# Optimization experiments

Hardware: AMD Instinct MI355X
Metric: run time of the kernel (lower is better)

## Reference

```python
import jax, jax.numpy as jnp
import numpy as np
import math

B, S, D, H = 4, 512, 1024, 16
DH = D // H
DQ = D // 4
MIN_STEPS, MAX_STEPS = 4, 12
THR = 1e-4


def lin(t, w, b):
    # torch Linear convention: w is (out, in)
    return jnp.einsum('...i,oi->...o', t, w) + b


def gelu(t):
    return jax.nn.gelu(t, approximate=False)  # torch nn.GELU() exact


def layernorm(t, g, b):
    m = t.mean(-1, keepdims=True)
    v = jnp.mean(jnp.square(t - m), axis=-1, keepdims=True)
    return (t - m) * jax.lax.rsqrt(v + 1e-5) * g + b


def _forward(h, x, ig_w1, ig_b1, ig_w2, ig_b2, wq, bq, wk, bk, wv, bv, wo, bo,
             g1_w1, g1_b1, g1_w2, g1_b2, gate_logits, ln_g, ln_b,
             sp_w1, sp_b1, sp_w2, sp_b2):
    # adaptive step count: steps = base + floor(sigmoid(MLP(mean_pool(h))).mean() * extra)
    pooled = h.mean(axis=1)  # (B, D)
    extra = jax.nn.sigmoid(lin(gelu(lin(pooled, sp_w1, sp_b1)), sp_w2, sp_b2)).mean()
    num_steps = jnp.minimum(
        MIN_STEPS + jnp.floor(extra * (MAX_STEPS - MIN_STEPS)).astype(jnp.int32), MAX_STEPS)

    gw = jax.nn.softmax(gate_logits)  # gate weights over the 3 gates
    scale = 1.0 / math.sqrt(DH)

    def step(carry, i):
        h, active = carry
        # G1 gate (G2/G3 multiply zero memory/expert outputs -> drop)
        G1 = jax.nn.sigmoid(lin(gelu(lin(h, g1_w1, g1_b1)), g1_w2, g1_b2)) * gw[0]
        # Phi: input-gated blend + raw multi-head self-attention
        gate = jax.nn.sigmoid(
            lin(gelu(lin(jnp.concatenate([h, x], axis=-1), ig_w1, ig_b1)), ig_w2, ig_b2))
        blended = gate * h + (1.0 - gate) * x
        q = lin(blended, wq, bq).reshape(B, S, H, DH)
        k = lin(blended, wk, bk).reshape(B, S, H, DH)
        v = lin(blended, wv, bv).reshape(B, S, H, DH)
        attn = jax.nn.softmax(jnp.einsum('bqhd,bkhd->bhqk', q, k) * scale, axis=-1)
        ctx = jnp.einsum('bhqk,bkhd->bqhd', attn, v).reshape(B, S, D)
        phi = lin(ctx, wo, bo)
        h_new = layernorm(h + G1 * phi, ln_g, ln_b)
        res = jnp.linalg.norm(h_new - h) / (jnp.linalg.norm(h) + 1e-8)
        act_i = active & (i < num_steps)
        h = jnp.where(act_i, h_new, h)
        active = act_i & jnp.logical_not((i >= MIN_STEPS) & (res < THR))
        return (h, active), None

    (h, _), _ = jax.lax.scan(step, (h, jnp.array(True)), jnp.arange(MAX_STEPS))
    return h


def setup_inputs() -> dict:
    key = jax.random.key(0)
    ks = jax.random.split(key, 16)
    f32 = jnp.float32

    def W(k, out_d, in_d):
        return jax.random.normal(k, (out_d, in_d), f32) * (1.0 / np.sqrt(in_d))

    return {
        'h': jax.random.normal(ks[0], (B, S, D), f32),
        'x': jax.random.normal(ks[1], (B, S, D), f32),
        # PhiLayer input_gate: Linear(2D, D/4) -> GELU -> Linear(D/4, D) -> Sigmoid
        'ig_w1': W(ks[2], DQ, 2 * D), 'ig_b1': jnp.zeros((DQ,), f32),
        'ig_w2': W(ks[3], D, DQ), 'ig_b2': jnp.zeros((D,), f32),
        # QKV / out projections (xavier-ish, zero bias)
        'wq': W(ks[4], D, D), 'bq': jnp.zeros((D,), f32),
        'wk': W(ks[5], D, D), 'bk': jnp.zeros((D,), f32),
        'wv': W(ks[6], D, D), 'bv': jnp.zeros((D,), f32),
        'wo': W(ks[7], D, D), 'bo': jnp.zeros((D,), f32),
        # Gating gate #1 MLP (only G1 contributes; memory/experts are zero)
        'g1_w1': W(ks[8], DQ, D), 'g1_b1': jnp.zeros((DQ,), f32),
        'g1_w2': W(ks[9], D, DQ), 'g1_b2': jnp.zeros((D,), f32),
        'gate_logits': jnp.ones((3,), f32),  # nn.Parameter(torch.ones(3))
        # LayerNorm
        'ln_g': jnp.ones((D,), f32), 'ln_b': jnp.zeros((D,), f32),
        # step predictor: Linear(D, D/4) -> GELU -> Linear(D/4, 1)
        'sp_w1': W(ks[10], DQ, D), 'sp_b1': jnp.zeros((DQ,), f32),
        'sp_w2': W(ks[11], 1, DQ), 'sp_b2': jnp.zeros((1,), f32),
    }


def reference(h, x, ig_w1, ig_b1, ig_w2, ig_b2, wq, bq, wk, bk, wv, bv, wo, bo,
              g1_w1, g1_b1, g1_w2, g1_b2, gate_logits, ln_g, ln_b,
              sp_w1, sp_b1, sp_w2, sp_b2):
    return _forward(h, x, ig_w1, ig_b1, ig_w2, ig_b2, wq, bq, wk, bk, wv, bv, wo, bo,
                    g1_w1, g1_b1, g1_w2, g1_b2, gate_logits, ln_g, ln_b,
                    sp_w1, sp_b1, sp_w2, sp_b2)
```

## Files before the change

kernel.cpp:

```cpp
#include <hip/hip_runtime.h>
#include <hip/hip_bf16.h>


#define B_   4
#define S_   512
#define D_   1024
#define H_   16
#define DH_  64
#define MSEQ 2048
#define GRID_ 512

typedef short short8 __attribute__((ext_vector_type(8)));
typedef float floatx4 __attribute__((ext_vector_type(4)));

static constexpr size_t OFF_H    = 0;
static constexpr size_t OFF_X    = 2097152;
static constexpr size_t OFF_HXB  = 4194304;
static constexpr size_t OFF_T2B  = 6291456;
static constexpr size_t OFF_T1B  = 6553600;
static constexpr size_t OFF_G1B  = 6815744;
static constexpr size_t OFF_QKVB = 7864320;
static constexpr size_t OFF_U    = 7864320;
static constexpr size_t OFF_CTXB = 11010048;
static constexpr size_t OFF_WARE = 12058624;
static constexpr size_t OFF_BIAS = 14811136;
static constexpr size_t OFF_POOL = 14817792;
static constexpr size_t OFF_SPT  = 14821888;
static constexpr size_t OFF_PPART= 14822912;
static constexpr size_t OFF_SCAL = 14888448;
static constexpr size_t OFF_XIG  = 14888960;

static constexpr int W_WIG1 = 0;
static constexpr int W_WIG2 = 524288;
static constexpr int W_WG1  = 786432;
static constexpr int W_WG2  = 1048576;
static constexpr int W_QKV  = 1310720;
static constexpr int W_WO   = 4456448;
static constexpr int W_TOT  = 5505024;
static constexpr int B_TOT  = 6656;

__device__ __forceinline__ float bf2f(unsigned int u) {
  return __uint_as_float((u & 0xFFFFu) << 16);
}
__device__ __forceinline__ short f2bs(float f) {
  __hip_bfloat16 b = __float2bfloat16(f);
  return *reinterpret_cast<short*>(&b);
}
__device__ __forceinline__ unsigned int pk2(float lo, float hi) {
  return (unsigned int)(unsigned short)f2bs(lo) | ((unsigned int)(unsigned short)f2bs(hi) << 16);
}
__device__ __forceinline__ float ldf(const void* p, size_t i, int f32m) {
  return f32m ? ((const float*)p)[i] : bf2f(((const unsigned short*)p)[i]);
}
__device__ __forceinline__ int f32mode(const void* lng) {
  return (((const unsigned int*)lng)[0] == 0x3F800000u) ? 1 : 0;
}
__device__ __forceinline__ float gelu_f(float x) {
  return 0.5f * x * (1.0f + erff(x * 0.70710678118654752440f));
}
__device__ __forceinline__ float sig_f(float x) {
  return 1.0f / (1.0f + expf(-x));
}
__device__ __forceinline__ void gl_lds16(const short* gp, short* lp) {
  __builtin_amdgcn_global_load_lds(
      (const __attribute__((address_space(1))) unsigned int*)gp,
      (__attribute__((address_space(3))) unsigned int*)lp, 16, 0, 0);
}
__device__ __forceinline__ float wave_sum(float v) {
  #pragma unroll
  for (int off = 32; off > 0; off >>= 1) v += __shfl_xor(v, off);
  return v;
}

struct RepackPtrs {
  const void* w[8];
  const void* b[8];
};

__global__ __launch_bounds__(256) void repack_all_kernel(
    const void* __restrict__ lng, RepackPtrs ps,
    short* __restrict__ wdst, float* __restrict__ bdst) {
  const int f32m = f32mode(lng);
  int i = blockIdx.x * 256 + threadIdx.x;
  if (i < W_TOT) {
    const int off[9] = {0, 524288, 786432, 1048576, 1310720, 2359296, 3407872, 4456448, W_TOT};
    int seg = 0;
    #pragma unroll
    for (int s = 1; s < 8; s++) seg += (i >= off[s]) ? 1 : 0;
    wdst[i] = f2bs(ldf(ps.w[seg], i - off[seg], f32m));
  } else if (i < W_TOT + B_TOT) {
    int j = i - W_TOT;
    const int off[9] = {0, 256, 1280, 1536, 2560, 3584, 4608, 5632, B_TOT};
    int seg = 0;
    #pragma unroll
    for (int s = 1; s < 8; s++) seg += (j >= off[s]) ? 1 : 0;
    bdst[j] = ldf(ps.b[seg], j - off[seg], f32m);
  }
}

__global__ __launch_bounds__(256) void cvt_in_kernel(
    const void* __restrict__ lng, const void* __restrict__ hb,
    const void* __restrict__ xb, float* __restrict__ h, float* __restrict__ x,
    short* __restrict__ hxb, int n) {
  int f32m = f32mode(lng);
  int i = blockIdx.x * 256 + threadIdx.x;
  if (i < n) {
    float hv = ldf(hb, i, f32m);
    float xv = ldf(xb, i, f32m);
    h[i] = hv;
    x[i] = xv;
    int row = i >> 10, col = i & 1023;
    hxb[(size_t)row * 2048 + col] = f2bs(hv);
    hxb[(size_t)row * 2048 + 1024 + col] = f2bs(xv);
  }
}

__global__ __launch_bounds__(256) void pool_s1_kernel(
    const float* __restrict__ H, float* __restrict__ part) {
  int b = blockIdx.x, c = blockIdx.y, tid = threadIdx.x;
  const float* p = H + ((size_t)b * S_ + c * 32) * D_;
  #pragma unroll
  for (int rep = 0; rep < 4; rep++) {
    int d = rep * 256 + tid;
    float s = 0.f;
    for (int r = 0; r < 32; r++) s += p[(size_t)r * D_ + d];
    part[((size_t)b * 16 + c) * D_ + d] = s;
  }
}
__global__ __launch_bounds__(256) void pool_s2_kernel(
    const float* __restrict__ part, float* __restrict__ pooled) {
  int i = blockIdx.x * 256 + threadIdx.x;
  int b = i >> 10, d = i & 1023;
  float s = 0.f;
  #pragma unroll
  for (int c = 0; c < 16; c++) s += part[((size_t)b * 16 + c) * D_ + d];
  pooled[i] = s * (1.0f / (float)S_);
}

__device__ __forceinline__ float blk_sum256(float v, float* sm, int tid) {
  #pragma unroll
  for (int off = 32; off > 0; off >>= 1) v += __shfl_xor(v, off);
  __syncthreads();
  if ((tid & 63) == 0) sm[tid >> 6] = v;
  __syncthreads();
  return sm[0] + sm[1] + sm[2] + sm[3];
}

__global__ __launch_bounds__(256) void sp1_kernel(
    const void* __restrict__ lng, const float* __restrict__ pooled,
    const void* __restrict__ w1, const void* __restrict__ b1,
    float* __restrict__ spt) {
  __shared__ float sm[4];
  const int f32m = f32mode(lng);
  int j = blockIdx.x, tid = threadIdx.x;
  float s[4] = {0.f, 0.f, 0.f, 0.f};
  #pragma unroll
  for (int r = 0; r < 4; r++) {
    int k = tid * 4 + r;
    float w = ldf(w1, (size_t)j * D_ + k, f32m);
    s[0] += pooled[k] * w;
    s[1] += pooled[1024 + k] * w;
    s[2] += pooled[2048 + k] * w;
    s[3] += pooled[3072 + k] * w;
  }
  #pragma unroll
  for (int b = 0; b < 4; b++) {
    float t = blk_sum256(s[b], sm, tid);
    __syncthreads();
    if (tid == 0) spt[b * 256 + j] = gelu_f(t + ldf(b1, j, f32m));
  }
}

__global__ __launch_bounds__(256) void sp2_kernel(
    const void* __restrict__ lng, const float* __restrict__ spt,
    const void* __restrict__ w2, const void* __restrict__ b2,
    const void* __restrict__ glog,
    int* __restrict__ num_steps, int* __restrict__ active, int* __restrict__ cur,
    float* __restrict__ gw0, float* __restrict__ ssd, float* __restrict__ ssh,
    int* __restrict__ cnt) {
  __shared__ float z[4];
  const int f32m = f32mode(lng);
  int tid = threadIdx.x;
  if (tid < 12) cnt[tid] = 0;
  int wave = tid >> 6, lane = tid & 63;
  {
    int b = wave;
    float s = spt[b * 256 + lane]       * ldf(w2, lane, f32m) +
              spt[b * 256 + lane + 64]  * ldf(w2, lane + 64, f32m) +
              spt[b * 256 + lane + 128] * ldf(w2, lane + 128, f32m) +
              spt[b * 256 + lane + 192] * ldf(w2, lane + 192, f32m);
    #pragma unroll
    for (int off = 32; off > 0; off >>= 1) s += __shfl_xor(s, off);
    if (lane == 0) z[b] = sig_f(s + ldf(b2, 0, f32m));
  }
  __syncthreads();
  if (tid == 0) {
    float extra = 0.25f * (z[0] + z[1] + z[2] + z[3]);
    int ns = 4 + (int)floorf(extra * 8.0f);
    if (ns > 12) ns = 12;
    *num_steps = ns;
    *active = 1;
    *cur = 1;
    *ssd = 0.f; *ssh = 0.f;
    float g0 = ldf(glog, 0, f32m);
    float g1 = ldf(glog, 1, f32m);
    float g2 = ldf(glog, 2, f32m);
    float mx = fmaxf(g0, fmaxf(g1, g2));
    float e0 = expf(g0 - mx), e1 = expf(g1 - mx), e2 = expf(g2 - mx);
    *gw0 = e0 / (e0 + e1 + e2);
  }
}

enum { EPI_NONE = 0, EPI_GELU = 1, EPI_SIGSCALE = 2, EPI_BLEND = 3, EPI_RESADD = 4,
       EPI_GELU_ADD = 5, EPI_F32NB = 6 };

template <int EPI, int BM, int BN>
__device__ __forceinline__ void mgemm_core(
    short* As, short* Bs,
    const short* __restrict__ A, int lda,
    const short* __restrict__ W, int ldw, const float* __restrict__ bias,
    int K, int N,
    float* __restrict__ Cf, short* __restrict__ Cb,
    const float* __restrict__ aux1, const float* __restrict__ aux2f,
    const short* __restrict__ aux2b, const float* __restrict__ scale_ptr,
    int m0, int n0) {
  constexpr int FM = (BM / 2) / 16;
  constexpr int FN = (BN / 2) / 16;
  constexpr int CPA = (BM / 16) / 4;
  constexpr int CPB = (BN / 16) / 4;
  const int tid = threadIdx.x;
  const int lane = tid & 63, wv_ = tid >> 6;
  const int wm = (wv_ >> 1) * (BM / 2), wn = (wv_ & 1) * (BN / 2);
  const int srow = lane >> 2, scol = (lane & 3) * 8;
  const int frow = lane & 15, fk = (lane >> 4) * 8;

  floatx4 acc[FM][FN];
  #pragma unroll
  for (int i = 0; i < FM; i++)
    #pragma unroll
    for (int j = 0; j < FN; j++) acc[i][j] = (floatx4){0.f, 0.f, 0.f, 0.f};

  for (int k0 = 0; k0 < K; k0 += 64) {
    __syncthreads();
    #pragma unroll
    for (int c = 0; c < CPA; c++) {
      int q = wv_ * CPA + c;
      const short* gp = A + (size_t)(m0 + q * 16 + srow) * lda + k0 + scol;
      gl_lds16(gp, As + q * 512);
      gl_lds16(gp + 32, As + BM * 32 + q * 512);
    }
    #pragma unroll
    for (int c = 0; c < CPB; c++) {
      int q = wv_ * CPB + c;
      const short* gp = W + (size_t)(n0 + q * 16 + srow) * ldw + k0 + scol;
      gl_lds16(gp, Bs + q * 512);
      gl_lds16(gp + 32, Bs + BN * 32 + q * 512);
    }
    __syncthreads();
    #pragma unroll
    for (int hlf = 0; hlf < 2; hlf++) {
      const short* Ah = As + hlf * BM * 32;
      const short* Bh = Bs + hlf * BN * 32;
      short8 a[FM], b[FN];
      #pragma unroll
      for (int i = 0; i < FM; i++)
        a[i] = *reinterpret_cast<const short8*>(&Ah[(wm + i * 16 + frow) * 32 + fk]);
      #pragma unroll
      for (int j = 0; j < FN; j++)
        b[j] = *reinterpret_cast<const short8*>(&Bh[(wn + j * 16 + frow) * 32 + fk]);
      #pragma unroll
      for (int i = 0; i < FM; i++)
        #pragma unroll
        for (int j = 0; j < FN; j++)
          acc[i][j] = __builtin_amdgcn_mfma_f32_16x16x32_bf16(a[i], b[j], acc[i][j], 0, 0, 0);
    }
  }

  float gwv = 0.f;
  if (EPI == EPI_SIGSCALE) gwv = *scale_ptr;
  const int rq = (lane >> 4) * 4;
  #pragma unroll
  for (int i = 0; i < FM; i++) {
    #pragma unroll
    for (int j = 0; j < FN; j++) {
      int n = n0 + wn + j * 16 + (lane & 15);
      float bv = (EPI == EPI_F32NB) ? 0.f : bias[n];
      #pragma unroll
      for (int r = 0; r < 4; r++) {
        int m = m0 + wm + i * 16 + rq + r;
        size_t off = (size_t)m * N + n;
        float v = acc[i][j][r] + bv;
        if (EPI == EPI_GELU) {
          Cb[off] = f2bs(gelu_f(v));
        } else if (EPI == EPI_GELU_ADD) {
          if (aux1) v += aux1[off];
          Cb[off] = f2bs(gelu_f(v));
        } else if (EPI == EPI_SIGSCALE) {
          Cb[off] = f2bs(sig_f(v) * gwv);
        } else if (EPI == EPI_BLEND) {
          float s = sig_f(v);
          Cb[off] = f2bs(s * aux1[off] + (1.f - s) * aux2f[off]);
        } else if (EPI == EPI_RESADD) {
          Cf[off] = aux1[off] + bf2f((unsigned short)aux2b[off]) * v;
        } else if (EPI == EPI_F32NB) {
          Cf[off] = v;
        } else {
          Cb[off] = f2bs(v);
        }
      }
    }
  }
}

template <int EPI, int BM, int BN>
__global__ __launch_bounds__(256) void mgemm(
    const int* __restrict__ flag, const short* __restrict__ A, int lda,
    const short* __restrict__ W, int ldw, const float* __restrict__ bias,
    int K, int N,
    float* __restrict__ Cf, short* __restrict__ Cb,
    const float* __restrict__ aux1, const float* __restrict__ aux2f,
    const short* __restrict__ aux2b, const float* __restrict__ scale_ptr) {
  if (flag && *flag == 0) return;
  __shared__ short As[BM * 64];
  __shared__ short Bs[BN * 64];
  mgemm_core<EPI, BM, BN>(As, Bs, A, lda, W, ldw, bias, K, N, Cf, Cb,
                          aux1, aux2f, aux2b, scale_ptr,
                          blockIdx.y * BM, blockIdx.x * BN);
}

__global__ __launch_bounds__(256) void gate1_kernel(
    const int* __restrict__ flag, const short* __restrict__ hxb,
    const short* __restrict__ warena, const float* __restrict__ biasA,
    short* __restrict__ t2b, short* __restrict__ t1b,
    const float* __restrict__ xig, int kz0) {
  if (*flag == 0) return;
  __shared__ short As[64 * 64];
  __shared__ short Bs[64 * 64];
  if (blockIdx.z == 0)
    mgemm_core<EPI_GELU_ADD, 64, 64>(As, Bs, hxb, 2048, warena + W_WIG1, 2048,
                                     biasA + 0, kz0, 256, nullptr, t2b, xig,
                                     nullptr, nullptr, nullptr,
                                     blockIdx.y * 64, blockIdx.x * 64);
  else
    mgemm_core<EPI_GELU, 64, 64>(As, Bs, hxb, 2048, warena + W_WG1, 1024,
                                 biasA + 1280, 1024, 256, nullptr, t1b, nullptr,
                                 nullptr, nullptr, nullptr,
                                 blockIdx.y * 64, blockIdx.x * 64);
}

__global__ __launch_bounds__(256) void gate2_kernel(
    const int* __restrict__ flag, const short* __restrict__ t2b,
    const short* __restrict__ t1b, const short* __restrict__ warena,
    const float* __restrict__ biasA, short* __restrict__ bldb,
    short* __restrict__ g1b, const float* __restrict__ h,
    const float* __restrict__ xf, const float* __restrict__ gw0) {
  if (*flag == 0) return;
  __shared__ short As[128 * 64];
  __shared__ short Bs[64 * 64];
  if (blockIdx.z == 0)
    mgemm_core<EPI_BLEND, 128, 64>(As, Bs, t2b, 256, warena + W_WIG2, 256,
                                   biasA + 256, 256, 1024, nullptr, bldb, h, xf,
                                   nullptr, nullptr, blockIdx.y * 128, blockIdx.x * 64);
  else
    mgemm_core<EPI_SIGSCALE, 128, 64>(As, Bs, t1b, 256, warena + W_WG2, 256,
                                      biasA + 1536, 256, 1024, nullptr, g1b,
                                      nullptr, nullptr, nullptr, gw0,
                                      blockIdx.y * 128, blockIdx.x * 64);
}

#define AP_ 72
__global__ __launch_bounds__(256) void attn_kernel(
    const int* __restrict__ flag, const short* __restrict__ qkv,
    short* __restrict__ ctxb) {
  if (*flag == 0) return;
  __shared__ short Ks[64 * AP_];
  __shared__ short Vt[64 * AP_];
  __shared__ short Ps[64 * AP_];
  const int tid = threadIdx.x;
  const int lane = tid & 63, wv = tid >> 6;
  const int ln15 = lane & 15, quad = lane >> 4;
  const int qt = blockIdx.x, hh = blockIdx.y, b = blockIdx.z;
  const int wm = wv * 16;
  const size_t rowbase = (size_t)b * S_;
  const int hcol = hh * DH_;
  const float scale = 0.125f;

  short8 qa[2];
  {
    const short* qp = qkv + (rowbase + qt * 64 + wm + ln15) * 3072 + hcol + quad * 8;
    qa[0] = *reinterpret_cast<const short8*>(qp);
    qa[1] = *reinterpret_cast<const short8*>(qp + 32);
  }
  const int skk = tid >> 2, scg = (tid & 3) * 16;

  float mrow[4] = {-1e30f, -1e30f, -1e30f, -1e30f};
  float lrow[4] = {0.f, 0.f, 0.f, 0.f};
  floatx4 accO[4];
  #pragma unroll
  for (int j = 0; j < 4; j++) accO[j] = (floatx4){0.f, 0.f, 0.f, 0.f};

  for (int kt = 0; kt < 8; kt++) {
    __syncthreads();
    {
      const short* gk = qkv + (rowbase + kt * 64 + skk) * 3072 + 1024 + hcol + scg;
      uint4 k0 = *reinterpret_cast<const uint4*>(gk);
      uint4 k1 = *reinterpret_cast<const uint4*>(gk + 8);
      *reinterpret_cast<uint4*>(&Ks[skk * AP_ + scg]) = k0;
      *reinterpret_cast<uint4*>(&Ks[skk * AP_ + scg + 8]) = k1;
      short8 v0 = *reinterpret_cast<const short8*>(gk + 1024);
      short8 v1 = *reinterpret_cast<const short8*>(gk + 1032);
      #pragma unroll
      for (int j = 0; j < 8; j++) Vt[(scg + j) * AP_ + skk] = v0[j];
      #pragma unroll
      for (int j = 0; j < 8; j++) Vt[(scg + 8 + j) * AP_ + skk] = v1[j];
    }
    __syncthreads();

    floatx4 sc[4];
    #pragma unroll
    for (int nf = 0; nf < 4; nf++) {
      short8 b0 = *reinterpret_cast<const short8*>(&Ks[(nf * 16 + ln15) * AP_ + quad * 8]);
      short8 b1 = *reinterpret_cast<const short8*>(&Ks[(nf * 16 + ln15) * AP_ + 32 + quad * 8]);
      floatx4 s = (floatx4){0.f, 0.f, 0.f, 0.f};
      s = __builtin_amdgcn_mfma_f32_16x16x32_bf16(qa[0], b0, s, 0, 0, 0);
      s = __builtin_amdgcn_mfma_f32_16x16x32_bf16(qa[1], b1, s, 0, 0, 0);
      sc[nf] = s;
    }

    float prob[4][4];
    #pragma unroll
    for (int r = 0; r < 4; r++) {
      float lm = fmaxf(fmaxf(sc[0][r], sc[1][r]), fmaxf(sc[2][r], sc[3][r])) * scale;
      lm = fmaxf(lm, __shfl_xor(lm, 1));
      lm = fmaxf(lm, __shfl_xor(lm, 2));
      lm = fmaxf(lm, __shfl_xor(lm, 4));
      lm = fmaxf(lm, __shfl_xor(lm, 8));
      float mn = fmaxf(mrow[r], lm);
      float alpha = expf(mrow[r] - mn);
      float ls = 0.f;
      #pragma unroll
      for (int nf = 0; nf < 4; nf++) {
        float p = expf(sc[nf][r] * scale - mn);
        prob[nf][r] = p;
        ls += p;
      }
      ls += __shfl_xor(ls, 1);
      ls += __shfl_xor(ls, 2);
      ls += __shfl_xor(ls, 4);
      ls += __shfl_xor(ls, 8);
      lrow[r] = lrow[r] * alpha + ls;
      mrow[r] = mn;
      #pragma unroll
      for (int df = 0; df < 4; df++) accO[df][r] *= alpha;
    }
    #pragma unroll
    for (int nf = 0; nf < 4; nf++)
      #pragma unroll
      for (int r = 0; r < 4; r++)
        Ps[(wm + quad * 4 + r) * AP_ + nf * 16 + ln15] = f2bs(prob[nf][r]);
    __syncthreads();

    short8 pa0 = *reinterpret_cast<const short8*>(&Ps[(wm + ln15) * AP_ + quad * 8]);
    short8 pa1 = *reinterpret_cast<const short8*>(&Ps[(wm + ln15) * AP_ + 32 + quad * 8]);
    #pragma unroll
    for (int df = 0; df < 4; df++) {
      short8 bv0 = *reinterpret_cast<const short8*>(&Vt[(df * 16 + ln15) * AP_ + quad * 8]);
      short8 bv1 = *reinterpret_cast<const short8*>(&Vt[(df * 16 + ln15) * AP_ + 32 + quad * 8]);
      accO[df] = __builtin_amdgcn_mfma_f32_16x16x32_bf16(pa0, bv0, accO[df], 0, 0, 0);
      accO[df] = __builtin_amdgcn_mfma_f32_16x16x32_bf16(pa1, bv1, accO[df], 0, 0, 0);
    }
  }

  float inv[4];
  #pragma unroll
  for (int r = 0; r < 4; r++) inv[r] = 1.0f / lrow[r];
  #pragma unroll
  for (int df = 0; df < 4; df++) {
    #pragma unroll
    for (int r = 0; r < 4; r++) {
      size_t off = (rowbase + qt * 64 + wm + quad * 4 + r) * 1024 + hcol + df * 16 + ln15;
      ctxb[off] = f2bs(accO[df][r] * inv[r]);
    }
  }
}

__global__ __launch_bounds__(256) void ln_kernel(
    int step_i, const int* __restrict__ flagp,
    const float* __restrict__ U, float* __restrict__ H, short* __restrict__ hxb,
    const void* __restrict__ g, const void* __restrict__ be,
    void* __restrict__ Out,
    float* __restrict__ ssd, float* __restrict__ ssh,
    int* __restrict__ active, int* __restrict__ cur,
    const int* __restrict__ num_steps, int* __restrict__ cnt) {
  const int flag = *flagp;
  const int f32m = f32mode(g);
  __shared__ float sdd[4], sdh[4];
  const int tid = threadIdx.x;
  const int wv = tid >> 6, lane = tid & 63;
  if (flag) {
    const int row = blockIdx.x * 4 + wv;
    const float4* u4 = reinterpret_cast<const float4*>(U + (size_t)row * D_);
    float4* h4 = reinterpret_cast<float4*>(H + (size_t)row * D_);
    float4 uv[4], hv[4];
    #pragma unroll
    for (int j = 0; j < 4; j++) uv[j] = u4[lane + 64 * j];
    #pragma unroll
    for (int j = 0; j < 4; j++) hv[j] = h4[lane + 64 * j];
    float s = 0.f;
    #pragma unroll
    for (int j = 0; j < 4; j++) s += (uv[j].x + uv[j].y) + (uv[j].z + uv[j].w);
    s = wave_sum(s);
    float mean = s * (1.0f / (float)D_);
    float4 d[4];
    float vv = 0.f;
    #pragma unroll
    for (int j = 0; j < 4; j++) {
      d[j].x = uv[j].x - mean; d[j].y = uv[j].y - mean;
      d[j].z = uv[j].z - mean; d[j].w = uv[j].w - mean;
      vv += d[j].x * d[j].x + d[j].y * d[j].y + d[j].z * d[j].z + d[j].w * d[j].w;
    }
    vv = wave_sum(vv);
    float rstd = rsqrtf(vv * (1.0f / (float)D_) + 1e-5f);
    float lsd = 0.f, lsh = 0.f;
    #pragma unroll
    for (int j = 0; j < 4; j++) {
      int c = (lane + 64 * j) * 4;
      float hn0 = d[j].x * rstd * ldf(g, c + 0, f32m) + ldf(be, c + 0, f32m);
      float hn1 = d[j].y * rstd * ldf(g, c + 1, f32m) + ldf(be, c + 1, f32m);
      float hn2 = d[j].z * rstd * ldf(g, c + 2, f32m) + ldf(be, c + 2, f32m);
      float hn3 = d[j].w * rstd * ldf(g, c + 3, f32m) + ldf(be, c + 3, f32m);
      float e0 = hn0 - hv[j].x, e1 = hn1 - hv[j].y, e2 = hn2 - hv[j].z, e3 = hn3 - hv[j].w;
      lsd += e0 * e0 + e1 * e1 + e2 * e2 + e3 * e3;
      lsh += hv[j].x * hv[j].x + hv[j].y * hv[j].y + hv[j].z * hv[j].z + hv[j].w * hv[j].w;
      float4 hnv = make_float4(hn0, hn1, hn2, hn3);
      h4[lane + 64 * j] = hnv;
      uint2 pw;
      pw.x = pk2(hn0, hn1);
      pw.y = pk2(hn2, hn3);
      *reinterpret_cast<uint2*>(hxb + (size_t)row * 2048 + c) = pw;
      if (f32m) {
        reinterpret_cast<float4*>(Out)[(size_t)row * 256 + lane + 64 * j] = hnv;
      } else {
        *reinterpret_cast<uint2*>((short*)Out + (size_t)row * 1024 + c) = pw;
      }
    }
    lsd = wave_sum(lsd);
    lsh = wave_sum(lsh);
    if (lane == 0) { sdd[wv] = lsd; sdh[wv] = lsh; }
    __syncthreads();
    if (tid == 0) {
      atomicAdd(ssd, (sdd[0] + sdd[1]) + (sdd[2] + sdd[3]));
      atomicAdd(ssh, (sdh[0] + sdh[1]) + (sdh[2] + sdh[3]));
    }
  }
  if (tid == 0) {
    __threadfence();
    int old = atomicAdd(&cnt[step_i], 1);
    if (old == (int)gridDim.x - 1) {
      if (flag && step_i >= 4) {
        float nd = atomicAdd(ssd, 0.0f);
        float nh = atomicAdd(ssh, 0.0f);
        float res = sqrtf(nd) / (sqrtf(nh) + 1e-8f);
        if (res < 1e-4f) *active = 0;
      }
      *cur = ((*active) && (step_i + 1 < *num_steps)) ? 1 : 0;
      *ssd = 0.f; *ssh = 0.f;
    }
  }
}

extern "C" void kernel_launch(void* const* d_in, const int* in_sizes, int n_in,
                              void* d_out, int out_size, void* d_ws, size_t ws_size,
                              hipStream_t stream) {
  (void)in_sizes; (void)n_in; (void)out_size;
  const void* h_in  = d_in[0];
  const void* x_in  = d_in[1];
  const void* glog  = d_in[18];
  const void* ln_g  = d_in[19];
  const void* ln_b  = d_in[20];
  const void* sp_w1 = d_in[21];
  const void* sp_b1 = d_in[22];
  const void* sp_w2 = d_in[23];
  const void* sp_b2 = d_in[24];

  RepackPtrs rp;
  rp.w[0] = d_in[2];  rp.w[1] = d_in[4];  rp.w[2] = d_in[14]; rp.w[3] = d_in[16];
  rp.w[4] = d_in[6];  rp.w[5] = d_in[8];  rp.w[6] = d_in[10]; rp.w[7] = d_in[12];
  rp.b[0] = d_in[3];  rp.b[1] = d_in[5];  rp.b[2] = d_in[15]; rp.b[3] = d_in[17];
  rp.b[4] = d_in[7];  rp.b[5] = d_in[9];  rp.b[6] = d_in[11]; rp.b[7] = d_in[13];

  float* wsf = (float*)d_ws;
  float* h      = wsf + OFF_H;
  float* xf     = wsf + OFF_X;
  short* hxb    = (short*)(wsf + OFF_HXB);
  short* t2b    = (short*)(wsf + OFF_T2B);
  short* t1b    = (short*)(wsf + OFF_T1B);
  short* g1b    = (short*)(wsf + OFF_G1B);
  short* qkvb   = (short*)(wsf + OFF_QKVB);
  float* u      = wsf + OFF_U;
  short* ctxb   = (short*)(wsf + OFF_CTXB);
  short* bldb   = ctxb;
  short* warena = (short*)(wsf + OFF_WARE);
  float* biasA  = wsf + OFF_BIAS;
  float* pooled = wsf + OFF_POOL;
  float* spt    = wsf + OFF_SPT;
  float* ppart  = wsf + OFF_PPART;
  float* xigf   = wsf + OFF_XIG;
  float* ssd    = wsf + OFF_SCAL + 0;
  float* ssh    = wsf + OFF_SCAL + 1;
  float* gw0    = wsf + OFF_SCAL + 2;
  int* ip        = (int*)(wsf + OFF_SCAL + 8);
  int* num_steps = ip + 0;
  int* active    = ip + 1;
  int* cur       = ip + 2;
  int* cnt       = ip + 4;

  const int NTOT = B_ * S_ * D_;

  const int use_xig = (ws_size >= (OFF_XIG + 524288) * sizeof(float)) ? 1 : 0;
  const int kz0 = use_xig ? 1024 : 2048;

  repack_all_kernel<<<(W_TOT + B_TOT + 255) / 256, 256, 0, stream>>>(ln_g, rp, warena, biasA);
  cvt_in_kernel<<<NTOT / 256, 256, 0, stream>>>(ln_g, h_in, x_in, h, xf, hxb, NTOT);
  if (use_xig) {
    mgemm<EPI_F32NB, 64, 64><<<dim3(4, 32), 256, 0, stream>>>(
        nullptr, hxb + 1024, 2048, warena + W_WIG1 + 1024, 2048, nullptr,
        1024, 256, xigf, nullptr, nullptr, nullptr, nullptr, nullptr);
  }
  pool_s1_kernel<<<dim3(4, 16), 256, 0, stream>>>(h, ppart);
  pool_s2_kernel<<<16, 256, 0, stream>>>(ppart, pooled);
  sp1_kernel<<<256, 256, 0, stream>>>(ln_g, pooled, sp_w1, sp_b1, spt);
  sp2_kernel<<<1, 256, 0, stream>>>(ln_g, spt, sp_w2, sp_b2, glog,
                                    num_steps, active, cur, gw0, ssd, ssh, cnt);

  for (int i = 0; i < 12; i++) {
    gate1_kernel<<<dim3(4, 32, 2), 256, 0, stream>>>(
        cur, hxb, warena, biasA, t2b, t1b, use_xig ? xigf : nullptr, kz0);
    gate2_kernel<<<dim3(16, 16, 2), 256, 0, stream>>>(cur, t2b, t1b, warena, biasA,
                                                      bldb, g1b, h, xf, gw0);
    mgemm<EPI_NONE, 128, 64><<<dim3(48, 16), 256, 0, stream>>>(
        cur, bldb, 1024, warena + W_QKV, 1024, biasA + 2560, 1024, 3072,
        nullptr, qkvb, nullptr, nullptr, nullptr, nullptr);
    attn_kernel<<<dim3(8, 16, 4), 256, 0, stream>>>(cur, qkvb, ctxb);
    mgemm<EPI_RESADD, 64, 64><<<dim3(16, 32), 256, 0, stream>>>(
        cur, ctxb, 1024, warena + W_WO, 1024, biasA + 5632, 1024, 1024,
        u, nullptr, h, nullptr, g1b, nullptr);
    ln_kernel<<<512, 256, 0, stream>>>(i, cur, u, h, hxb, ln_g, ln_b, d_out,
                                       ssd, ssh, active, cur, num_steps, cnt);
  }
}
```

Measured before the change: 1.201 ms.

## Enlarge attention query tile to 128 rows with transposed MFMA and packed stores

The attention kernel now runs 8 waves per block over 128 query rows, so each K/V tile staged in LDS is shared by twice as many waves and global K/V reloads are halved. The per-wave P buffer no longer needs a block barrier before it is read back, so one __syncthreads is dropped. The PV MFMA operand order is swapped to produce a transposed accumulator, with alpha and the row sums redistributed by lane shuffles, which allows 8-byte packed bf16 stores of the context. The trade-off is half as many blocks in the grid, which means less parallelism across CUs.

Result: no change. 1.214 ms (+1.0%).

```diff
diff --git a/kernel.cpp b/kernel.cpp
--- a/kernel.cpp
+++ b/kernel.cpp
@@ -369,13 +369,13 @@
 }
 
 #define AP_ 72
-__global__ __launch_bounds__(256) void attn_kernel(
+__global__ __launch_bounds__(512) void attn_kernel(
     const int* __restrict__ flag, const short* __restrict__ qkv,
     short* __restrict__ ctxb) {
   if (*flag == 0) return;
   __shared__ short Ks[64 * AP_];
   __shared__ short Vt[64 * AP_];
-  __shared__ short Ps[64 * AP_];
+  __shared__ short Ps[128 * AP_];
   const int tid = threadIdx.x;
   const int lane = tid & 63, wv = tid >> 6;
   const int ln15 = lane & 15, quad = lane >> 4;
@@ -384,14 +384,16 @@
   const size_t rowbase = (size_t)b * S_;
   const int hcol = hh * DH_;
   const float scale = 0.125f;
+  const int srcl = ((ln15 >> 2) << 4) + ln15;
+  const int rsel = ln15 & 3;
 
   short8 qa[2];
   {
-    const short* qp = qkv + (rowbase + qt * 64 + wm + ln15) * 3072 + hcol + quad * 8;
+    const short* qp = qkv + (rowbase + qt * 128 + wm + ln15) * 3072 + hcol + quad * 8;
     qa[0] = *reinterpret_cast<const short8*>(qp);
     qa[1] = *reinterpret_cast<const short8*>(qp + 32);
   }
-  const int skk = tid >> 2, scg = (tid & 3) * 16;
+  const int skk = tid >> 3, scg = (tid & 7) * 8;
 
   float mrow[4] = {-1e30f, -1e30f, -1e30f, -1e30f};
   float lrow[4] = {0.f, 0.f, 0.f, 0.f};
@@ -404,15 +406,10 @@
     {
       const short* gk = qkv + (rowbase + kt * 64 + skk) * 3072 + 1024 + hcol + scg;
       uint4 k0 = *reinterpret_cast<const uint4*>(gk);
-      uint4 k1 = *reinterpret_cast<const uint4*>(gk + 8);
       *reinterpret_cast<uint4*>(&Ks[skk * AP_ + scg]) = k0;
-      *reinterpret_cast<uint4*>(&Ks[skk * AP_ + scg + 8]) = k1;
       short8 v0 = *reinterpret_cast<const short8*>(gk + 1024);
-      short8 v1 = *reinterpret_cast<const short8*>(gk + 1032);
       #pragma unroll
       for (int j = 0; j < 8; j++) Vt[(scg + j) * AP_ + skk] = v0[j];
-      #pragma unroll
-      for (int j = 0; j < 8; j++) Vt[(scg + 8 + j) * AP_ + skk] = v1[j];
     }
     __syncthreads();
 
@@ -428,6 +425,7 @@
     }
 
     float prob[4][4];
+    float alpha[4];
     #pragma unroll
     for (int r = 0; r < 4; r++) {
       float lm = fmaxf(fmaxf(sc[0][r], sc[1][r]), fmaxf(sc[2][r], sc[3][r])) * scale;
@@ -436,7 +434,7 @@
       lm = fmaxf(lm, __shfl_xor(lm, 4));
       lm = fmaxf(lm, __shfl_xor(lm, 8));
       float mn = fmaxf(mrow[r], lm);
-      float alpha = expf(mrow[r] - mn);
+      alpha[r] = expf(mrow[r] - mn);
       float ls = 0.f;
       #pragma unroll
       for (int nf = 0; nf < 4; nf++) {
@@ -448,17 +446,24 @@
       ls += __shfl_xor(ls, 2);
       ls += __shfl_xor(ls, 4);
       ls += __shfl_xor(ls, 8);
-      lrow[r] = lrow[r] * alpha + ls;
+      lrow[r] = lrow[r] * alpha[r] + ls;
       mrow[r] = mn;
-      #pragma unroll
-      for (int df = 0; df < 4; df++) accO[df][r] *= alpha;
-    }
+    }
+    float a0 = __shfl(alpha[0], srcl);
+    float a1 = __shfl(alpha[1], srcl);
+    float a2 = __shfl(alpha[2], srcl);
+    float a3 = __shfl(alpha[3], srcl);
+    float aq = (rsel == 0) ? a0 : (rsel == 1) ? a1 : (rsel == 2) ? a2 : a3;
+    #pragma unroll
+    for (int df = 0; df < 4; df++)
+      #pragma unroll
+      for (int r = 0; r < 4; r++) accO[df][r] *= aq;
+
     #pragma unroll
     for (int nf = 0; nf < 4; nf++)
       #pragma unroll
       for (int r = 0; r < 4; r++)
         Ps[(wm + quad * 4 + r) * AP_ + nf * 16 + ln15] = f2bs(prob[nf][r]);
-    __syncthreads();
 
     short8 pa0 = *reinterpret_cast<const short8*>(&Ps[(wm + ln15) * AP_ + quad * 8]);
     short8 pa1 = *reinterpret_cast<const short8*>(&Ps[(wm + ln15) * AP_ + 32 + quad * 8]);
@@ -466,21 +471,24 @@
     for (int df = 0; df < 4; df++) {
       short8 bv0 = *reinterpret_cast<const short8*>(&Vt[(df * 16 + ln15) * AP_ + quad * 8]);
       short8 bv1 = *reinterpret_cast<const short8*>(&Vt[(df * 16 + ln15) * AP_ + 32 + quad * 8]);
-      accO[df] = __builtin_amdgcn_mfma_f32_16x16x32_bf16(pa0, bv0, accO[df], 0, 0, 0);
-      accO[df] = __builtin_amdgcn_mfma_f32_16x16x32_bf16(pa1, bv1, accO[df], 0, 0, 0);
-    }
-  }
-
-  float inv[4];
-  #pragma unroll
-  for (int r = 0; r < 4; r++) inv[r] = 1.0f / lrow[r];
+      accO[df] = __builtin_amdgcn_mfma_f32_16x16x32_bf16(bv0, pa0, accO[df], 0, 0, 0);
+      accO[df] = __builtin_amdgcn_mfma_f32_16x16x32_bf16(bv1, pa1, accO[df], 0, 0, 0);
+    }
+  }
+
+  float l0 = __shfl(lrow[0], srcl);
+  float l1 = __shfl(lrow[1], srcl);
+  float l2 = __shfl(lrow[2], srcl);
+  float l3 = __shfl(lrow[3], srcl);
+  float lq = (rsel == 0) ? l0 : (rsel == 1) ? l1 : (rsel == 2) ? l2 : l3;
+  float invq = 1.0f / lq;
+  const size_t rowoff = (rowbase + qt * 128 + wm + ln15) * 1024 + hcol;
   #pragma unroll
   for (int df = 0; df < 4; df++) {
-    #pragma unroll
-    for (int r = 0; r < 4; r++) {
-      size_t off = (rowbase + qt * 64 + wm + quad * 4 + r) * 1024 + hcol + df * 16 + ln15;
-      ctxb[off] = f2bs(accO[df][r] * inv[r]);
-    }
+    uint2 pw;
+    pw.x = pk2(accO[df][0] * invq, accO[df][1] * invq);
+    pw.y = pk2(accO[df][2] * invq, accO[df][3] * invq);
+    *reinterpret_cast<uint2*>(ctxb + rowoff + df * 16 + quad * 4) = pw;
   }
 }
 
@@ -641,7 +649,7 @@
     mgemm<EPI_NONE, 128, 64><<<dim3(48, 16), 256, 0, stream>>>(
         cur, bldb, 1024, warena + W_QKV, 1024, biasA + 2560, 1024, 3072,
         nullptr, qkvb, nullptr, nullptr, nullptr, nullptr);
-    attn_kernel<<<dim3(8, 16, 4), 256, 0, stream>>>(cur, qkvb, ctxb);
+    attn_kernel<<<dim3(4, 16, 4), 512, 0, stream>>>(cur, qkvb, ctxb);
     mgemm<EPI_RESADD, 64, 64><<<dim3(16, 32), 256, 0, stream>>>(
         cur, ctxb, 1024, warena + W_WO, 1024, biasA + 5632, 1024, 1024,
         u, nullptr, h, nullptr, g1b, nullptr);
```

## Fuse both gate MLP layers into one kernel with on-chip hidden activations

Applied to the files above, without the earlier changes.

Merges the two gate GEMM kernels (the first layer with GELU, then the second layer with the blend or sigmoid-scale epilogue) into one kernel. Each block handles 16 rows and keeps the 256-wide GELU hidden activations in swizzled LDS instead of writing them to global memory. This removes one launch per step and the intermediate round trip. In exchange, each block reloads the full W1 and W2 weights for only 16 rows, and the grid shrinks to 256 blocks with large LDS, which lowers weight reuse and may lower occupancy.

Result: slower. 1.372 ms (+14.2%).

```diff
diff --git a/kernel.cpp b/kernel.cpp
--- a/kernel.cpp
+++ b/kernel.cpp
@@ -328,44 +328,123 @@
                           blockIdx.y * BM, blockIdx.x * BN);
 }
 
-__global__ __launch_bounds__(256) void gate1_kernel(
+__global__ __launch_bounds__(256) void gate12_kernel(
     const int* __restrict__ flag, const short* __restrict__ hxb,
     const short* __restrict__ warena, const float* __restrict__ biasA,
-    short* __restrict__ t2b, short* __restrict__ t1b,
-    const float* __restrict__ xig, int kz0) {
+    short* __restrict__ bldb, short* __restrict__ g1b,
+    const float* __restrict__ h, const float* __restrict__ xf,
+    const float* __restrict__ gw0, const float* __restrict__ xig, int kz0) {
   if (*flag == 0) return;
-  __shared__ short As[64 * 64];
-  __shared__ short Bs[64 * 64];
-  if (blockIdx.z == 0)
-    mgemm_core<EPI_GELU_ADD, 64, 64>(As, Bs, hxb, 2048, warena + W_WIG1, 2048,
-                                     biasA + 0, kz0, 256, nullptr, t2b, xig,
-                                     nullptr, nullptr, nullptr,
-                                     blockIdx.y * 64, blockIdx.x * 64);
-  else
-    mgemm_core<EPI_GELU, 64, 64>(As, Bs, hxb, 2048, warena + W_WG1, 1024,
-                                 biasA + 1280, 1024, 256, nullptr, t1b, nullptr,
-                                 nullptr, nullptr, nullptr,
-                                 blockIdx.y * 64, blockIdx.x * 64);
-}
-
-__global__ __launch_bounds__(256) void gate2_kernel(
-    const int* __restrict__ flag, const short* __restrict__ t2b,
-    const short* __restrict__ t1b, const short* __restrict__ warena,
-    const float* __restrict__ biasA, short* __restrict__ bldb,
-    short* __restrict__ g1b, const float* __restrict__ h,
-    const float* __restrict__ xf, const float* __restrict__ gw0) {
-  if (*flag == 0) return;
-  __shared__ short As[128 * 64];
-  __shared__ short Bs[64 * 64];
-  if (blockIdx.z == 0)
-    mgemm_core<EPI_BLEND, 128, 64>(As, Bs, t2b, 256, warena + W_WIG2, 256,
-                                   biasA + 256, 256, 1024, nullptr, bldb, h, xf,
-                                   nullptr, nullptr, blockIdx.y * 128, blockIdx.x * 64);
-  else
-    mgemm_core<EPI_SIGSCALE, 128, 64>(As, Bs, t1b, 256, warena + W_WG2, 256,
-                                      biasA + 1536, 256, 1024, nullptr, g1b,
-                                      nullptr, nullptr, nullptr, gw0,
-                                      blockIdx.y * 128, blockIdx.x * 64);
+  __shared__ short As[16 * 64];
+  __shared__ short Bs[512 * 64];
+  __shared__ short T2[16 * 256];
+  const int z = (int)blockIdx.y;
+  const int m0 = (int)blockIdx.x * 16;
+  const int tid = threadIdx.x;
+  const int lane = tid & 63, wv = tid >> 6;
+  const int srow = lane >> 2, scol = (lane & 3) * 8;
+  const int frow = lane & 15, quad = lane >> 4, fk = quad * 8;
+  const int rq = quad * 4, ln15 = lane & 15;
+
+  const short* W1 = warena + (z ? W_WG1 : W_WIG1);
+  const int ldw1 = z ? 1024 : 2048;
+  const int K1 = z ? 1024 : kz0;
+  const int b1off = z ? 1280 : 0;
+
+  floatx4 acc1[4];
+  #pragma unroll
+  for (int j = 0; j < 4; j++) acc1[j] = (floatx4){0.f, 0.f, 0.f, 0.f};
+
+  for (int k0 = 0; k0 < K1; k0 += 64) {
+    __syncthreads();
+    if (wv == 0) {
+      const short* gp = hxb + (size_t)(m0 + srow) * 2048 + k0 + scol;
+      gl_lds16(gp, As);
+      gl_lds16(gp + 32, As + 512);
+    }
+    #pragma unroll
+    for (int c = 0; c < 4; c++) {
+      int q = wv * 4 + c;
+      const short* gp = W1 + (size_t)(q * 16 + srow) * ldw1 + k0 + scol;
+      gl_lds16(gp, Bs + q * 512);
+      gl_lds16(gp + 32, Bs + 256 * 32 + q * 512);
+    }
+    __syncthreads();
+    #pragma unroll
+    for (int hlf = 0; hlf < 2; hlf++) {
+      const short* Ah = As + hlf * 512;
+      const short* Bh = Bs + hlf * 256 * 32;
+      short8 a = *reinterpret_cast<const short8*>(&Ah[frow * 32 + fk]);
+      #pragma unroll
+      for (int j = 0; j < 4; j++) {
+        short8 b = *reinterpret_cast<const short8*>(&Bh[(wv * 64 + j * 16 + frow) * 32 + fk]);
+        acc1[j] = __builtin_amdgcn_mfma_f32_16x16x32_bf16(a, b, acc1[j], 0, 0, 0);
+      }
+    }
+  }
+  __syncthreads();
+  #pragma unroll
+  for (int j = 0; j < 4; j++) {
+    int n = wv * 64 + j * 16 + ln15;
+    float bv = biasA[b1off + n];
+    #pragma unroll
+    for (int r = 0; r < 4; r++) {
+      int m = rq + r;
+      float v = acc1[j][r] + bv;
+      if (z == 0 && xig) v += xig[(size_t)(m0 + m) * 256 + n];
+      T2[m * 256 + (n ^ ((m & 7) << 3))] = f2bs(gelu_f(v));
+    }
+  }
+
+  const short* W2 = warena + (z ? W_WG2 : W_WIG2);
+  const int b2off = z ? 1536 : 256;
+  float gwv = z ? *gw0 : 0.f;
+  #pragma unroll
+  for (int g = 0; g < 2; g++) {
+    floatx4 acc2[8];
+    #pragma unroll
+    for (int j = 0; j < 8; j++) acc2[j] = (floatx4){0.f, 0.f, 0.f, 0.f};
+    for (int kk = 0; kk < 256; kk += 64) {
+      __syncthreads();
+      #pragma unroll
+      for (int c = 0; c < 8; c++) {
+        int q = wv * 8 + c;
+        const short* gp = W2 + (size_t)(g * 512 + q * 16 + srow) * 256 + kk + scol;
+        gl_lds16(gp, Bs + q * 512);
+        gl_lds16(gp + 32, Bs + 512 * 32 + q * 512);
+      }
+      __syncthreads();
+      #pragma unroll
+      for (int hlf = 0; hlf < 2; hlf++) {
+        int kbase = kk + hlf * 32 + fk;
+        short8 a = *reinterpret_cast<const short8*>(
+            &T2[frow * 256 + (kbase ^ ((frow & 7) << 3))]);
+        const short* Bh = Bs + hlf * 512 * 32;
+        #pragma unroll
+        for (int j = 0; j < 8; j++) {
+          short8 b = *reinterpret_cast<const short8*>(&Bh[(wv * 128 + j * 16 + frow) * 32 + fk]);
+          acc2[j] = __builtin_amdgcn_mfma_f32_16x16x32_bf16(a, b, acc2[j], 0, 0, 0);
+        }
+      }
+    }
+    #pragma unroll
+    for (int j = 0; j < 8; j++) {
+      int n = g * 512 + wv * 128 + j * 16 + ln15;
+      float bv = biasA[b2off + n];
+      #pragma unroll
+      for (int r = 0; r < 4; r++) {
+        int m = m0 + rq + r;
+        size_t off = (size_t)m * 1024 + n;
+        float v = acc2[j][r] + bv;
+        if (z == 0) {
+          float s = sig_f(v);
+          bldb[off] = f2bs(s * h[off] + (1.f - s) * xf[off]);
+        } else {
+          g1b[off] = f2bs(sig_f(v) * gwv);
+        }
+      }
+    }
+  }
 }
 
 #define AP_ 72
@@ -593,8 +672,6 @@
   float* h      = wsf + OFF_H;
   float* xf     = wsf + OFF_X;
   short* hxb    = (short*)(wsf + OFF_HXB);
-  short* t2b    = (short*)(wsf + OFF_T2B);
-  short* t1b    = (short*)(wsf + OFF_T1B);
   short* g1b    = (short*)(wsf + OFF_G1B);
   short* qkvb   = (short*)(wsf + OFF_QKVB);
   float* u      = wsf + OFF_U;
@@ -634,10 +711,9 @@
                                     num_steps, active, cur, gw0, ssd, ssh, cnt);
 
   for (int i = 0; i < 12; i++) {
-    gate1_kernel<<<dim3(4, 32, 2), 256, 0, stream>>>(
-        cur, hxb, warena, biasA, t2b, t1b, use_xig ? xigf : nullptr, kz0);
-    gate2_kernel<<<dim3(16, 16, 2), 256, 0, stream>>>(cur, t2b, t1b, warena, biasA,
-                                                      bldb, g1b, h, xf, gw0);
+    gate12_kernel<<<dim3(128, 2), 256, 0, stream>>>(
+        cur, hxb, warena, biasA, bldb, g1b, h, xf, gw0,
+        use_xig ? xigf : nullptr, kz0);
     mgemm<EPI_NONE, 128, 64><<<dim3(48, 16), 256, 0, stream>>>(
         cur, bldb, 1024, warena + W_QKV, 1024, biasA + 2560, 1024, 3072,
         nullptr, qkvb, nullptr, nullptr, nullptr, nullptr);
```
